# Performance work log

Measured on AMD Instinct MI355X. Metric: run time of the kernel, lower is better.

The kernel has to match this reference:

```python
import jax, jax.numpy as jnp
import numpy as np

N_POST = 50000   # dense_shape[0], number of postsynaptic neurons
N_IN = 17400     # dense_shape[1], number of input (LGN) units
NNZ = 1000000    # number of synapses
N_SYN_BASIS = 5  # receptor basis functions
N_SYN_TYPES = 10


def setup_inputs() -> dict:
    key = jax.random.key(0)
    k1, k2, k3, k4, k5, k6 = jax.random.split(key, 6)
    inp = jax.random.normal(k1, (1, 64, N_IN), dtype=jnp.float32)
    rows = jax.random.randint(k2, (NNZ,), 0, N_POST)
    cols = jax.random.randint(k3, (NNZ,), 0, N_IN)
    indices = jnp.stack([rows, cols], axis=1).astype(jnp.int64)  # [nnz, 2]
    input_weights = jax.random.normal(k4, (NNZ,), dtype=jnp.float32)
    synaptic_weights = jax.random.uniform(k5, (N_SYN_TYPES, N_SYN_BASIS), dtype=jnp.float32)
    syn_ids = jax.random.randint(k6, (NNZ,), 0, N_SYN_TYPES).astype(jnp.int64)
    return {"inp": inp, "indices": indices, "input_weights": input_weights,
            "synaptic_weights": synaptic_weights, "syn_ids": syn_ids}


def reference(inp, indices, input_weights, synaptic_weights, syn_ids):
    B, T, n_in = inp.shape
    tokens = B * T
    x = inp.reshape(tokens, n_in)              # flatten (batch, time)
    rows = indices[:, 0]
    cols = indices[:, 1]
    # per-synapse receptor factors: synaptic_weights[syn_ids] -> [nnz, n_basis]
    factors = jnp.take(synaptic_weights, syn_ids, axis=0)
    # gather presynaptic activity once for all receptor bases: [nnz, tokens]
    g = jnp.take(x.T, cols, axis=0)
    outs = []
    for r in range(N_SYN_BASIS):
        vals = input_weights * factors[:, r]                      # [nnz]
        contrib = g * vals[:, None]                               # [nnz, tokens]
        # sparse-dense matmul == segment-sum over destination rows
        out_r = jax.ops.segment_sum(contrib, rows, num_segments=N_POST)  # [n_post, tokens]
        outs.append(out_r)
    i_in = jnp.stack(outs, axis=0)                                # [n_basis, n_post, tokens]
    # tf.transpose of 3D reverses dims -> [tokens, n_post, n_basis]
    out = jnp.transpose(i_in, (2, 1, 0)).reshape(B, T, N_POST * N_SYN_BASIS)
    return out
```

## Files before the change

kernel.cpp:

```cpp
#include <hip/hip_runtime.h>
#include <hip/hip_fp16.h>

#define N_POST 50000
#define N_IN   17400
#define NNZ_E  1000000
#define T_DIM  64
#define R_DIM  5
#define NT_DIM 10

#define BROWS  256
#define NBUCK  ((N_POST + BROWS - 1) / BROWS)
#define EPB    4096
#define NBLK1  ((NNZ_E + EPB - 1) / EPB)
#define CAP    64
#define FCAP   5632
#define CAPR   7168
#define CTILES ((N_IN + 63) / 64)
#define RECBUF_N 1024

static __device__ __forceinline__ unsigned pack2h(float a, float b) {
    __half2 h = __floats2half2_rn(a, b);
    return *reinterpret_cast<unsigned*>(&h);
}

__global__ __launch_bounds__(1024) void k_ts(const float* __restrict__ x,
                                             __half* __restrict__ xT,
                                             const int2* __restrict__ idx2,
                                             const float* __restrict__ iw,
                                             const int* __restrict__ sid,
                                             unsigned short* __restrict__ cnt,
                                             uint2* __restrict__ rec1) {
    __shared__ float tile[64][65];
    int bb = blockIdx.x;
    int tid = threadIdx.x;
    if (bb < CTILES) {
        int c0 = bb * 64;
        int l = tid & 63, w = tid >> 6;
        #pragma unroll
        for (int i = 0; i < 4; ++i) {
            int t = i * 16 + w;
            int c = c0 + l;
            tile[l][t] = (c < N_IN) ? x[t * N_IN + c] : 0.f;
        }
        __syncthreads();
        #pragma unroll
        for (int i = 0; i < 4; ++i) {
            int cc = i * 16 + w;
            int c = c0 + cc;
            if (c < N_IN) xT[c * 64 + l] = __float2half(tile[cc][l]);
        }
        return;
    }
    int* lcur = (int*)&tile[0][0];
    for (int i = tid; i < NBUCK; i += 1024) lcur[i] = 0;
    __syncthreads();
    int blk = bb - CTILES;
    int base = blk * EPB;
    int n = min(EPB, NNZ_E - base);
    for (int i = tid; i < n; i += 1024) {
        int2 rc = idx2[base + i];
        unsigned bk = (unsigned)rc.x >> 8;
        int pos = atomicAdd(&lcur[bk], 1);
        unsigned xx = (unsigned)rc.y | ((unsigned)sid[base + i] << 15)
                    | ((unsigned)(rc.x & 255) << 19);
        rec1[(bk * NBLK1 + blk) * CAP + pos] =
            make_uint2(xx, __float_as_uint(iw[base + i]));
    }
    __syncthreads();
    for (int i = tid; i < NBUCK; i += 1024)
        cnt[i * NBLK1 + blk] = (unsigned short)lcur[i];
}

__global__ __launch_bounds__(512) void k_fine(const uint2* __restrict__ rec1,
                                              const unsigned short* __restrict__ cnt,
                                              const float* __restrict__ S,
                                              uint4* __restrict__ rec,
                                              int* __restrict__ rstart,
                                              int* __restrict__ plen) {
    __shared__ uint2 lrec[FCAP];
    __shared__ int scnt[256];
    __shared__ int soff[256];
    __shared__ int lhist[BROWS];
    __shared__ int lsc[BROWS];
    __shared__ int lcur[BROWS];
    __shared__ float s_S[NT_DIM * R_DIM];
    int t = threadIdx.x;
    int b = blockIdx.x;
    int pbase = b * CAPR;
    if (t < NT_DIM * R_DIM) s_S[t] = S[t];
    int cv = 0;
    if (t < 256) {
        cv = (t < NBLK1) ? (int)cnt[b * NBLK1 + t] : 0;
        scnt[t] = cv;
        soff[t] = cv;
        lhist[t] = 0;
    }
    __syncthreads();
    for (int off = 1; off < 256; off <<= 1) {
        int u = 0;
        if (t < 256 && t >= off) u = soff[t - off];
        __syncthreads();
        if (t < 256) soff[t] += u;
        __syncthreads();
    }
    if (t < 256) soff[t] -= cv;
    __syncthreads();
    const uint2* srcb = rec1 + (size_t)b * NBLK1 * CAP;
    for (int slot = t; slot < NBLK1 * CAP; slot += 512) {
        int cell = slot >> 6;
        int j = slot & 63;
        if (j < scnt[cell]) lrec[soff[cell] + j] = srcb[slot];
    }
    int nrec = soff[255] + scnt[255];
    __syncthreads();
    for (int i = t; i < nrec; i += 512)
        atomicAdd(&lhist[(lrec[i].x >> 19) & 255], 1);
    __syncthreads();
    if (t < 256) soff[t] = (lhist[t] + 3) & ~3;
    __syncthreads();
    int v = 0, vp = 0;
    if (t < 256) {
        v = lhist[t];
        vp = max(soff[t], soff[t ^ 1]);
        lsc[t] = vp;
    }
    __syncthreads();
    for (int off = 1; off < 256; off <<= 1) {
        int u = 0;
        if (t < 256 && t >= off) u = lsc[t - off];
        __syncthreads();
        if (t < 256) lsc[t] += u;
        __syncthreads();
    }
    if (t < 256) {
        int exclp = lsc[t] - vp;
        int p = b * BROWS + t;
        if (p < N_POST) { rstart[p] = pbase + exclp; plen[p] = vp; }
        lcur[t] = exclp;
    }
    __syncthreads();
    for (int i = t; i < nrec; i += 512) {
        uint2 rc = lrec[i];
        int r = (rc.x >> 19) & 255;
        int pos = atomicAdd(&lcur[r], 1);
        unsigned col = rc.x & 0x7FFF;
        const float* f = &s_S[((rc.x >> 15) & 0xF) * R_DIM];
        float w = __uint_as_float(rc.y);
        uint4 r4;
        r4.x = col << 7;
        r4.y = pack2h(w * f[0], w * f[1]);
        r4.z = pack2h(w * f[2], w * f[3]);
        r4.w = pack2h(w * f[4], 0.f);
        rec[pbase + pos] = r4;
    }
    if (t < 256) {
        int exclp = lsc[t] - vp;
        for (int u = v; u < vp; ++u)
            rec[pbase + exclp + u] = make_uint4(0, 0, 0, 0);
    }
}

#define FMAREC(Rk, Xk)                                                              \
    do {                                                                            \
        unsigned x_ = (Xk);                                                         \
        unsigned w01_ = (Rk).y, w23_ = (Rk).z, w4_ = (Rk).w;                        \
        asm("v_fma_mix_f32 %0, %1, %2, %0 op_sel:[0,0,0] op_sel_hi:[1,1,0]"         \
            : "+v"(a0e) : "v"(x_), "v"(w01_));                                      \
        asm("v_fma_mix_f32 %0, %1, %2, %0 op_sel:[1,0,0] op_sel_hi:[1,1,0]"         \
            : "+v"(a0o) : "v"(x_), "v"(w01_));                                      \
        asm("v_fma_mix_f32 %0, %1, %2, %0 op_sel:[0,1,0] op_sel_hi:[1,1,0]"         \
            : "+v"(a1e) : "v"(x_), "v"(w01_));                                      \
        asm("v_fma_mix_f32 %0, %1, %2, %0 op_sel:[1,1,0] op_sel_hi:[1,1,0]"         \
            : "+v"(a1o) : "v"(x_), "v"(w01_));                                      \
        asm("v_fma_mix_f32 %0, %1, %2, %0 op_sel:[0,0,0] op_sel_hi:[1,1,0]"         \
            : "+v"(a2e) : "v"(x_), "v"(w23_));                                      \
        asm("v_fma_mix_f32 %0, %1, %2, %0 op_sel:[1,0,0] op_sel_hi:[1,1,0]"         \
            : "+v"(a2o) : "v"(x_), "v"(w23_));                                      \
        asm("v_fma_mix_f32 %0, %1, %2, %0 op_sel:[0,1,0] op_sel_hi:[1,1,0]"         \
            : "+v"(a3e) : "v"(x_), "v"(w23_));                                      \
        asm("v_fma_mix_f32 %0, %1, %2, %0 op_sel:[1,1,0] op_sel_hi:[1,1,0]"         \
            : "+v"(a3o) : "v"(x_), "v"(w23_));                                      \
        asm("v_fma_mix_f32 %0, %1, %2, %0 op_sel:[0,0,0] op_sel_hi:[1,1,0]"         \
            : "+v"(a4e) : "v"(x_), "v"(w4_));                                       \
        asm("v_fma_mix_f32 %0, %1, %2, %0 op_sel:[1,0,0] op_sel_hi:[1,1,0]"         \
            : "+v"(a4o) : "v"(x_), "v"(w4_));                                       \
    } while (0)

#define LOADSET(P0, P1, P2, P3, XX0, XX1, XX2, XX3, q)                              \
    do {                                                                            \
        P0 = (q)[0]; P1 = (q)[1]; P2 = (q)[2]; P3 = (q)[3];                         \
        XX0 = *(const unsigned*)(xb + (P0.x + lane4));                              \
        XX1 = *(const unsigned*)(xb + (P1.x + lane4));                              \
        XX2 = *(const unsigned*)(xb + (P2.x + lane4));                              \
        XX3 = *(const unsigned*)(xb + (P3.x + lane4));                              \
    } while (0)

#define ROWBODY(RP)                                                                 \
    do {                                                                            \
        if (ng > 0) {                                                               \
            LOADSET(A0, A1, A2, A3, XA0, XA1, XA2, XA3, (RP));                      \
            int g = 1;                                                              \
            for (; g + 2 <= ng; g += 2) {                                           \
                LOADSET(B0, B1, B2, B3, XB0, XB1, XB2, XB3, (RP) + (g << 2));       \
                FMAREC(A0, XA0); FMAREC(A1, XA1);                                   \
                FMAREC(A2, XA2); FMAREC(A3, XA3);                                   \
                LOADSET(A0, A1, A2, A3, XA0, XA1, XA2, XA3, (RP) + ((g + 1) << 2)); \
                FMAREC(B0, XB0); FMAREC(B1, XB1);                                   \
                FMAREC(B2, XB2); FMAREC(B3, XB3);                                   \
            }                                                                       \
            if (g < ng) {                                                           \
                LOADSET(B0, B1, B2, B3, XB0, XB1, XB2, XB3, (RP) + (g << 2));       \
                FMAREC(A0, XA0); FMAREC(A1, XA1);                                   \
                FMAREC(A2, XA2); FMAREC(A3, XA3);                                   \
                FMAREC(B0, XB0); FMAREC(B1, XB1);                                   \
                FMAREC(B2, XB2); FMAREC(B3, XB3);                                   \
            } else {                                                                \
                FMAREC(A0, XA0); FMAREC(A1, XA1);                                   \
                FMAREC(A2, XA2); FMAREC(A3, XA3);                                   \
            }                                                                       \
        }                                                                           \
    } while (0)

__global__ __launch_bounds__(256, 4) void k_phase2(
        const __half* __restrict__ xT, const int* __restrict__ rstart,
        const int* __restrict__ plen, const uint4* __restrict__ rec,
        float* __restrict__ out) {
    __shared__ float o_lds[T_DIM * 81];
    __shared__ uint4 recbuf[RECBUF_N];
    const char* xb = (const char*)xT;
    int tid = threadIdx.x;
    int wave = tid >> 6, lane = tid & 63;
    int half = lane >> 5;
    int lane4 = (lane & 31) * 4;
    int p0 = blockIdx.x * 16;
    int start0 = rstart[p0];
    int nblk = rstart[p0 + 15] + plen[p0 + 15] - start0;
    bool uselds = (nblk <= RECBUF_N);
    if (uselds) {
        for (int i = tid; i < nblk; i += 256) recbuf[i] = rec[start0 + i];
    }
    __syncthreads();
    #pragma unroll
    for (int h = 0; h < 2; ++h) {
        int pa = p0 + wave * 4 + h * 2;
        int myrow = pa + half;
        int ih = rstart[myrow];
        int ng = __builtin_amdgcn_readfirstlane(plen[pa]) >> 2;
        float a0e = 0.f, a0o = 0.f, a1e = 0.f, a1o = 0.f, a2e = 0.f;
        float a2o = 0.f, a3e = 0.f, a3o = 0.f, a4e = 0.f, a4o = 0.f;
        uint4 A0, A1, A2, A3, B0, B1, B2, B3;
        unsigned XA0, XA1, XA2, XA3, XB0, XB1, XB2, XB3;
        if (uselds) {
            const uint4* rp = recbuf + (ih - start0);
            ROWBODY(rp);
        } else {
            const uint4* rp = rec + ih;
            ROWBODY(rp);
        }
        int rowl = wave * 4 + h * 2 + half;
        int t0 = (lane & 31) * 2;
        float* d0 = &o_lds[t0 * 81 + rowl * 5];
        d0[0] = a0e; d0[1] = a1e; d0[2] = a2e; d0[3] = a3e; d0[4] = a4e;
        float* d1 = &o_lds[(t0 + 1) * 81 + rowl * 5];
        d1[0] = a0o; d1[1] = a1o; d1[2] = a2o; d1[3] = a3o; d1[4] = a4o;
    }
    __syncthreads();
    int base5 = blockIdx.x * 80;
    for (int i2 = tid; i2 < T_DIM * 80; i2 += 256) {
        int t = i2 / 80;
        int j = i2 - t * 80;
        out[(size_t)t * (N_POST * R_DIM) + base5 + j] = o_lds[t * 81 + j];
    }
}

extern "C" void kernel_launch(void* const* d_in, const int* in_sizes, int n_in,
                              void* d_out, int out_size, void* d_ws, size_t ws_size,
                              hipStream_t stream) {
    const float* inp  = (const float*)d_in[0];
    const int2*  idx2 = (const int2*)d_in[1];
    const float* iw   = (const float*)d_in[2];
    const float* S    = (const float*)d_in[3];
    const int*   sid  = (const int*)d_in[4];
    float* out = (float*)d_out;

    char* ws = (char*)d_ws;
    size_t off = 0;
    auto alloc = [&](size_t bytes) -> void* {
        void* p = ws + off;
        off += (bytes + 255) & ~(size_t)255;
        return p;
    };
    __half* xT            = (__half*)alloc((size_t)N_IN * T_DIM * 2);
    unsigned short* cnt   = (unsigned short*)alloc((size_t)NBUCK * NBLK1 * 2);
    int*   rstart         = (int*)alloc((size_t)N_POST * 4);
    int*   plen           = (int*)alloc((size_t)N_POST * 4);
    uint2* rec1           = (uint2*)alloc((size_t)NBUCK * NBLK1 * CAP * 8);
    uint4* rec            = (uint4*)alloc((size_t)NBUCK * CAPR * 16);

    k_ts<<<CTILES + NBLK1, 1024, 0, stream>>>(inp, xT, idx2, iw, sid, cnt, rec1);
    k_fine<<<NBUCK, 512, 0, stream>>>(rec1, cnt, S, rec, rstart, plen);
    k_phase2<<<N_POST / 16, 256, 0, stream>>>(xT, rstart, plen, rec, out);
}
```

Baseline: 67.79 us.

## Process four rows per wave with four tokens per lane in phase2

Phase 2 now maps 16 lanes to each of four rows, so one wave covers four rows in a single pass instead of two rows per pass over two passes. Each lane loads 8 bytes (four half tokens) per record and keeps 20 accumulators. Row padding in the bucketing kernel is widened to the maximum over groups of four rows so all four rows in a wave share one loop count, and the bucket capacity grows to fit that extra padding. This is meant to halve the per-wave loop overhead and record loads and to issue wider x loads, at the cost of more registers and more padded zero records.

```diff
diff --git a/kernel.cpp b/kernel.cpp
--- a/kernel.cpp
+++ b/kernel.cpp
@@ -14,7 +14,7 @@
 #define NBLK1  ((NNZ_E + EPB - 1) / EPB)
 #define CAP    64
 #define FCAP   5632
-#define CAPR   7168
+#define CAPR   8192
 #define CTILES ((N_IN + 63) / 64)
 #define RECBUF_N 1024
 
@@ -121,7 +121,8 @@
     int v = 0, vp = 0;
     if (t < 256) {
         v = lhist[t];
-        vp = max(soff[t], soff[t ^ 1]);
+        int b4 = t & ~3;
+        vp = max(max(soff[b4], soff[b4 + 1]), max(soff[b4 + 2], soff[b4 + 3]));
         lsc[t] = vp;
     }
     __syncthreads();
@@ -160,65 +161,74 @@
     }
 }
 
-#define FMAREC(Rk, Xk)                                                              \
-    do {                                                                            \
-        unsigned x_ = (Xk);                                                         \
-        unsigned w01_ = (Rk).y, w23_ = (Rk).z, w4_ = (Rk).w;                        \
-        asm("v_fma_mix_f32 %0, %1, %2, %0 op_sel:[0,0,0] op_sel_hi:[1,1,0]"         \
-            : "+v"(a0e) : "v"(x_), "v"(w01_));                                      \
-        asm("v_fma_mix_f32 %0, %1, %2, %0 op_sel:[1,0,0] op_sel_hi:[1,1,0]"         \
-            : "+v"(a0o) : "v"(x_), "v"(w01_));                                      \
-        asm("v_fma_mix_f32 %0, %1, %2, %0 op_sel:[0,1,0] op_sel_hi:[1,1,0]"         \
-            : "+v"(a1e) : "v"(x_), "v"(w01_));                                      \
-        asm("v_fma_mix_f32 %0, %1, %2, %0 op_sel:[1,1,0] op_sel_hi:[1,1,0]"         \
-            : "+v"(a1o) : "v"(x_), "v"(w01_));                                      \
-        asm("v_fma_mix_f32 %0, %1, %2, %0 op_sel:[0,0,0] op_sel_hi:[1,1,0]"         \
-            : "+v"(a2e) : "v"(x_), "v"(w23_));                                      \
-        asm("v_fma_mix_f32 %0, %1, %2, %0 op_sel:[1,0,0] op_sel_hi:[1,1,0]"         \
-            : "+v"(a2o) : "v"(x_), "v"(w23_));                                      \
-        asm("v_fma_mix_f32 %0, %1, %2, %0 op_sel:[0,1,0] op_sel_hi:[1,1,0]"         \
-            : "+v"(a3e) : "v"(x_), "v"(w23_));                                      \
-        asm("v_fma_mix_f32 %0, %1, %2, %0 op_sel:[1,1,0] op_sel_hi:[1,1,0]"         \
-            : "+v"(a3o) : "v"(x_), "v"(w23_));                                      \
-        asm("v_fma_mix_f32 %0, %1, %2, %0 op_sel:[0,0,0] op_sel_hi:[1,1,0]"         \
-            : "+v"(a4e) : "v"(x_), "v"(w4_));                                       \
-        asm("v_fma_mix_f32 %0, %1, %2, %0 op_sel:[1,0,0] op_sel_hi:[1,1,0]"         \
-            : "+v"(a4o) : "v"(x_), "v"(w4_));                                       \
+#define FMX(acc, xs, xsel, ws, wsel)                                               \
+    asm("v_fma_mix_f32 %0, %1, %2, %0 op_sel:[" #xsel "," #wsel ",0] "             \
+        "op_sel_hi:[1,1,0]" : "+v"(acc) : "v"(xs), "v"(ws))
+
+#define FMAREC20(Rk, Xk)                                                           \
+    do {                                                                           \
+        unsigned xlo_ = (Xk).x, xhi_ = (Xk).y;                                     \
+        unsigned w01_ = (Rk).y, w23_ = (Rk).z, w4_ = (Rk).w;                       \
+        FMX(a00, xlo_, 0, w01_, 0); FMX(a01, xlo_, 0, w01_, 1);                    \
+        FMX(a02, xlo_, 0, w23_, 0); FMX(a03, xlo_, 0, w23_, 1);                    \
+        FMX(a04, xlo_, 0, w4_,  0);                                               \
+        FMX(a10, xhi_, 1, w01_, 0); FMX(a11, xhi_, 1, w01_, 1);                    \
+        FMX(a12, xhi_, 1, w23_, 0); FMX(a13, xhi_, 1, w23_, 1);                    \
+        FMX(a14, xhi_, 1, w4_,  0);                                               \
     } while (0)
 
-#define LOADSET(P0, P1, P2, P3, XX0, XX1, XX2, XX3, q)                              \
-    do {                                                                            \
-        P0 = (q)[0]; P1 = (q)[1]; P2 = (q)[2]; P3 = (q)[3];                         \
-        XX0 = *(const unsigned*)(xb + (P0.x + lane4));                              \
-        XX1 = *(const unsigned*)(xb + (P1.x + lane4));                              \
-        XX2 = *(const unsigned*)(xb + (P2.x + lane4));                              \
-        XX3 = *(const unsigned*)(xb + (P3.x + lane4));                              \
+#define FMAREC20B(Rk, Xk)                                                          \
+    do {                                                                           \
+        unsigned xlo_ = (Xk).x, xhi_ = (Xk).y;                                     \
+        unsigned w01_ = (Rk).y, w23_ = (Rk).z, w4_ = (Rk).w;                       \
+        FMX(a00, xlo_, 0, w01_, 0); FMX(a01, xlo_, 0, w01_, 1);                    \
+        FMX(a02, xlo_, 0, w23_, 0); FMX(a03, xlo_, 0, w23_, 1);                    \
+        FMX(a04, xlo_, 0, w4_,  0);                                               \
+        FMX(a10, xlo_, 1, w01_, 0); FMX(a11, xlo_, 1, w01_, 1);                    \
+        FMX(a12, xlo_, 1, w23_, 0); FMX(a13, xlo_, 1, w23_, 1);                    \
+        FMX(a14, xlo_, 1, w4_,  0);                                               \
+        FMX(a20, xhi_, 0, w01_, 0); FMX(a21, xhi_, 0, w01_, 1);                    \
+        FMX(a22, xhi_, 0, w23_, 0); FMX(a23, xhi_, 0, w23_, 1);                    \
+        FMX(a24, xhi_, 0, w4_,  0);                                               \
+        FMX(a30, xhi_, 1, w01_, 0); FMX(a31, xhi_, 1, w01_, 1);                    \
+        FMX(a32, xhi_, 1, w23_, 0); FMX(a33, xhi_, 1, w23_, 1);                    \
+        FMX(a34, xhi_, 1, w4_,  0);                                               \
     } while (0)
 
-#define ROWBODY(RP)                                                                 \
-    do {                                                                            \
-        if (ng > 0) {                                                               \
-            LOADSET(A0, A1, A2, A3, XA0, XA1, XA2, XA3, (RP));                      \
-            int g = 1;                                                              \
-            for (; g + 2 <= ng; g += 2) {                                           \
-                LOADSET(B0, B1, B2, B3, XB0, XB1, XB2, XB3, (RP) + (g << 2));       \
-                FMAREC(A0, XA0); FMAREC(A1, XA1);                                   \
-                FMAREC(A2, XA2); FMAREC(A3, XA3);                                   \
-                LOADSET(A0, A1, A2, A3, XA0, XA1, XA2, XA3, (RP) + ((g + 1) << 2)); \
-                FMAREC(B0, XB0); FMAREC(B1, XB1);                                   \
-                FMAREC(B2, XB2); FMAREC(B3, XB3);                                   \
-            }                                                                       \
-            if (g < ng) {                                                           \
-                LOADSET(B0, B1, B2, B3, XB0, XB1, XB2, XB3, (RP) + (g << 2));       \
-                FMAREC(A0, XA0); FMAREC(A1, XA1);                                   \
-                FMAREC(A2, XA2); FMAREC(A3, XA3);                                   \
-                FMAREC(B0, XB0); FMAREC(B1, XB1);                                   \
-                FMAREC(B2, XB2); FMAREC(B3, XB3);                                   \
-            } else {                                                                \
-                FMAREC(A0, XA0); FMAREC(A1, XA1);                                   \
-                FMAREC(A2, XA2); FMAREC(A3, XA3);                                   \
-            }                                                                       \
-        }                                                                           \
+#define LOADSET4(P0, P1, P2, P3, XX0, XX1, XX2, XX3, q_)                           \
+    do {                                                                           \
+        P0 = (q_)[0]; P1 = (q_)[1]; P2 = (q_)[2]; P3 = (q_)[3];                    \
+        XX0 = *(const uint2*)(xb + (P0.x + s8));                                   \
+        XX1 = *(const uint2*)(xb + (P1.x + s8));                                   \
+        XX2 = *(const uint2*)(xb + (P2.x + s8));                                   \
+        XX3 = *(const uint2*)(xb + (P3.x + s8));                                   \
+    } while (0)
+
+#define ROWBODY4(RP)                                                               \
+    do {                                                                           \
+        if (ng > 0) {                                                              \
+            LOADSET4(A0, A1, A2, A3, XA0, XA1, XA2, XA3, (RP));                    \
+            int g = 1;                                                             \
+            for (; g + 2 <= ng; g += 2) {                                          \
+                LOADSET4(B0, B1, B2, B3, XB0, XB1, XB2, XB3, (RP) + (g << 2));     \
+                FMAREC20B(A0, XA0); FMAREC20B(A1, XA1);                            \
+                FMAREC20B(A2, XA2); FMAREC20B(A3, XA3);                            \
+                LOADSET4(A0, A1, A2, A3, XA0, XA1, XA2, XA3,                       \
+                         (RP) + ((g + 1) << 2));                                   \
+                FMAREC20B(B0, XB0); FMAREC20B(B1, XB1);                            \
+                FMAREC20B(B2, XB2); FMAREC20B(B3, XB3);                            \
+            }                                                                      \
+            if (g < ng) {                                                          \
+                LOADSET4(B0, B1, B2, B3, XB0, XB1, XB2, XB3, (RP) + (g << 2));     \
+                FMAREC20B(A0, XA0); FMAREC20B(A1, XA1);                            \
+                FMAREC20B(A2, XA2); FMAREC20B(A3, XA3);                            \
+                FMAREC20B(B0, XB0); FMAREC20B(B1, XB1);                            \
+                FMAREC20B(B2, XB2); FMAREC20B(B3, XB3);                            \
+            } else {                                                               \
+                FMAREC20B(A0, XA0); FMAREC20B(A1, XA1);                            \
+                FMAREC20B(A2, XA2); FMAREC20B(A3, XA3);                            \
+            }                                                                      \
+        }                                                                          \
     } while (0)
 
 __global__ __launch_bounds__(256, 4) void k_phase2(
@@ -230,8 +240,8 @@
     const char* xb = (const char*)xT;
     int tid = threadIdx.x;
     int wave = tid >> 6, lane = tid & 63;
-    int half = lane >> 5;
-    int lane4 = (lane & 31) * 4;
+    int q = lane >> 4, s = lane & 15;
+    int s8 = s * 8;
     int p0 = blockIdx.x * 16;
     int start0 = rstart[p0];
     int nblk = rstart[p0 + 15] + plen[p0 + 15] - start0;
@@ -240,29 +250,33 @@
         for (int i = tid; i < nblk; i += 256) recbuf[i] = rec[start0 + i];
     }
     __syncthreads();
-    #pragma unroll
-    for (int h = 0; h < 2; ++h) {
-        int pa = p0 + wave * 4 + h * 2;
-        int myrow = pa + half;
-        int ih = rstart[myrow];
-        int ng = __builtin_amdgcn_readfirstlane(plen[pa]) >> 2;
-        float a0e = 0.f, a0o = 0.f, a1e = 0.f, a1o = 0.f, a2e = 0.f;
-        float a2o = 0.f, a3e = 0.f, a3o = 0.f, a4e = 0.f, a4o = 0.f;
-        uint4 A0, A1, A2, A3, B0, B1, B2, B3;
-        unsigned XA0, XA1, XA2, XA3, XB0, XB1, XB2, XB3;
-        if (uselds) {
-            const uint4* rp = recbuf + (ih - start0);
-            ROWBODY(rp);
-        } else {
-            const uint4* rp = rec + ih;
-            ROWBODY(rp);
-        }
-        int rowl = wave * 4 + h * 2 + half;
-        int t0 = (lane & 31) * 2;
-        float* d0 = &o_lds[t0 * 81 + rowl * 5];
-        d0[0] = a0e; d0[1] = a1e; d0[2] = a2e; d0[3] = a3e; d0[4] = a4e;
-        float* d1 = &o_lds[(t0 + 1) * 81 + rowl * 5];
-        d1[0] = a0o; d1[1] = a1o; d1[2] = a2o; d1[3] = a3o; d1[4] = a4o;
+    int pa = p0 + wave * 4;
+    int myrow = pa + q;
+    int ih = rstart[myrow];
+    int ng = __builtin_amdgcn_readfirstlane(plen[pa]) >> 2;
+    float a00 = 0.f, a01 = 0.f, a02 = 0.f, a03 = 0.f, a04 = 0.f;
+    float a10 = 0.f, a11 = 0.f, a12 = 0.f, a13 = 0.f, a14 = 0.f;
+    float a20 = 0.f, a21 = 0.f, a22 = 0.f, a23 = 0.f, a24 = 0.f;
+    float a30 = 0.f, a31 = 0.f, a32 = 0.f, a33 = 0.f, a34 = 0.f;
+    uint4 A0, A1, A2, A3, B0, B1, B2, B3;
+    uint2 XA0, XA1, XA2, XA3, XB0, XB1, XB2, XB3;
+    if (uselds) {
+        const uint4* rp = recbuf + (ih - start0);
+        ROWBODY4(rp);
+    } else {
+        const uint4* rp = rec + ih;
+        ROWBODY4(rp);
+    }
+    int rowl = wave * 4 + q;
+    {
+        float* d0 = &o_lds[(4 * s + 0) * 81 + rowl * 5];
+        d0[0] = a00; d0[1] = a01; d0[2] = a02; d0[3] = a03; d0[4] = a04;
+        float* d1 = &o_lds[(4 * s + 1) * 81 + rowl * 5];
+        d1[0] = a10; d1[1] = a11; d1[2] = a12; d1[3] = a13; d1[4] = a14;
+        float* d2 = &o_lds[(4 * s + 2) * 81 + rowl * 5];
+        d2[0] = a20; d2[1] = a21; d2[2] = a22; d2[3] = a23; d2[4] = a24;
+        float* d3 = &o_lds[(4 * s + 3) * 81 + rowl * 5];
+        d3[0] = a30; d3[1] = a31; d3[2] = a32; d3[3] = a33; d3[4] = a34;
     }
     __syncthreads();
     int base5 = blockIdx.x * 80;
```

New measurement: 65.04 us. -4.1%, faster.
